# Performance work log

Measured on AMD Instinct MI355X. Metric: run time of the kernel, lower is better.

Reference implementation:

```python
import jax, jax.numpy as jnp
import numpy as np

N_NODES = 100000
N_EDGES = 1600000


def setup_inputs() -> dict:
    key = jax.random.key(0)
    ks = jax.random.split(key, 8)
    in_f, hid, out_c = 128, 128, 64
    return {
        "x": jax.random.normal(ks[0], (N_NODES, in_f), jnp.float32),
        "W_self1": jax.random.normal(ks[1], (in_f, hid), jnp.float32) * 0.05,
        "W_neigh1": jax.random.normal(ks[2], (in_f, hid), jnp.float32) * 0.05,
        "b1": jnp.zeros((hid,), jnp.float32),
        "W_self2": jax.random.normal(ks[3], (hid, out_c), jnp.float32) * 0.05,
        "W_neigh2": jax.random.normal(ks[4], (hid, out_c), jnp.float32) * 0.05,
        "b2": jnp.zeros((out_c,), jnp.float32),
        "src": jax.random.randint(ks[5], (N_EDGES,), 0, N_NODES, jnp.int32),
        "dst": jax.random.randint(ks[6], (N_EDGES,), 0, N_NODES, jnp.int32),
    }


def _sage_conv(h, src, dst, inv_deg, W_self, W_neigh, b):
    # mean aggregation over incoming neighbors: gather + segment-sum + normalize
    agg = jax.ops.segment_sum(h[src], dst, num_segments=N_NODES) * inv_deg  # [N, d]
    return h @ W_self + agg @ W_neigh + b


def reference(x, W_self1, W_neigh1, b1, W_self2, W_neigh2, b2, src, dst):
    # in-degree, clamped to 1 as in DGL SAGEConv
    deg = jax.ops.segment_sum(jnp.ones((N_EDGES,), x.dtype), dst, num_segments=N_NODES)
    inv_deg = (1.0 / jnp.maximum(deg, 1.0))[:, None]  # [N, 1]

    h1 = _sage_conv(x, src, dst, inv_deg, W_self1, W_neigh1, b1)      # conv1
    h1_relu = jax.nn.relu(h1)
    h2 = _sage_conv(h1_relu, src, dst, inv_deg, W_self2, W_neigh2, b2)  # conv2
    # original returns (h, middle_feat=[h1, relu(h1), h2])
    return (h2, h1, h1_relu, h2)
```

## Files before the change

kernel.cpp:

```cpp
#include <hip/hip_runtime.h>
#include <hip/hip_bf16.h>


#define NFEAT 128

typedef __bf16 bf16x8 __attribute__((ext_vector_type(8)));
typedef float  f32x4  __attribute__((ext_vector_type(4)));
typedef unsigned short ushort8v __attribute__((ext_vector_type(8)));

static __device__ inline unsigned short f2bf(float f) {
    union { float f; unsigned int u; } v; v.f = f;
    unsigned int u = v.u;
    unsigned int r = (u + 0x7FFFu + ((u >> 16) & 1u)) >> 16;
    return (unsigned short)r;
}
static __device__ inline float bf2f(unsigned short h) {
    union { unsigned int u; float f; } v; v.u = ((unsigned int)h) << 16;
    return v.f;
}

__global__ __launch_bounds__(256) void k_deg(const int* __restrict__ dst,
                                             int* __restrict__ deg,
                                             int E, int P) {
    int part = blockIdx.x & 7;
    int slice = blockIdx.x >> 3;
    int nslices = gridDim.x >> 3;
    int per = (E + nslices - 1) / nslices;
    int beg = slice * per;
    int end = beg + per; if (end > E) end = E;
    int lo = part * P;
    int hi = lo + P;
    for (int e = beg + threadIdx.x; e < end; e += 256) {
        int d = dst[e];
        if (d >= lo && d < hi) atomicAdd(&deg[d], 1);
    }
}

__global__ __launch_bounds__(256) void k_scan1(const int* __restrict__ deg,
                                               int* __restrict__ escan,
                                               int* __restrict__ bsum, int n) {
    __shared__ int ws4[4];
    int tid = threadIdx.x;
    int base = blockIdx.x * 1024 + tid * 4;
    int d[4];
    #pragma unroll
    for (int j = 0; j < 4; ++j) d[j] = (base + j < n) ? deg[base + j] : 0;
    int s = d[0] + d[1] + d[2] + d[3];
    int lane = tid & 63, wid = tid >> 6;
    int incl = s;
    #pragma unroll
    for (int off = 1; off < 64; off <<= 1) {
        int t = __shfl_up(incl, off, 64);
        if (lane >= off) incl += t;
    }
    if (lane == 63) ws4[wid] = incl;
    __syncthreads();
    int wbase = 0;
    #pragma unroll
    for (int w = 0; w < 4; ++w) if (w < wid) wbase += ws4[w];
    int run = wbase + incl - s;
    #pragma unroll
    for (int j = 0; j < 4; ++j) {
        if (base + j < n) escan[base + j] = run;
        run += d[j];
    }
    if (tid == 255) bsum[blockIdx.x] = run;
}

__global__ __launch_bounds__(1024) void k_scan2(int* __restrict__ bsum, int nb) {
    __shared__ int ws16[16];
    int tid = threadIdx.x;
    int lane = tid & 63, wid = tid >> 6;
    int v = (tid < nb) ? bsum[tid] : 0;
    int incl = v;
    #pragma unroll
    for (int off = 1; off < 64; off <<= 1) {
        int t = __shfl_up(incl, off, 64);
        if (lane >= off) incl += t;
    }
    if (lane == 63) ws16[wid] = incl;
    __syncthreads();
    int wbase = 0;
    for (int w = 0; w < 16; ++w) if (w < wid) wbase += ws16[w];
    if (tid < nb) bsum[tid] = wbase + incl - v;
}

__global__ __launch_bounds__(256) void k_scan3(const int* __restrict__ deg,
                                               const int* __restrict__ escan,
                                               const int* __restrict__ bsum,
                                               int* __restrict__ offs,
                                               int* __restrict__ cursor,
                                               float* __restrict__ invd, int n) {
    int tid = threadIdx.x;
    int base = blockIdx.x * 1024 + tid * 4;
    int bb = bsum[blockIdx.x];
    #pragma unroll
    for (int j = 0; j < 4; ++j) {
        int i = base + j;
        if (i < n) {
            int d = deg[i];
            int off = escan[i] + bb;
            offs[i] = off;
            cursor[i] = off;
            invd[i] = 1.0f / fmaxf((float)d, 1.0f);
            if (i == n - 1) offs[n] = off + d;
        }
    }
}

__global__ __launch_bounds__(256) void k_prep(const float* __restrict__ x,
                                              unsigned short* __restrict__ xb,
                                              const float* __restrict__ Ws1,
                                              const float* __restrict__ Wn1,
                                              unsigned short* __restrict__ wb1,
                                              const float* __restrict__ Ws2,
                                              const float* __restrict__ Wn2,
                                              unsigned short* __restrict__ wb2,
                                              int total4, int C) {
    int b = blockIdx.x;
    if (b < C) {
        int i = b * 256 + threadIdx.x;
        if (i >= total4) return;
        float4 v = *(const float4*)(x + (size_t)i * 4);
        ushort4 o;
        o.x = f2bf(v.x); o.y = f2bf(v.y); o.z = f2bf(v.z); o.w = f2bf(v.w);
        *(ushort4*)(xb + (size_t)i * 4) = o;
    } else if (b < C + 128) {
        int idx = (b - C) * 256 + threadIdx.x;
        int j = idx & 7, lane = (idx >> 3) & 63, ct = (idx >> 9) & 7, ks = idx >> 12;
        int k = ks * 32 + ((lane >> 4) & 3) * 8 + j;
        int n = ct * 16 + (lane & 15);
        float v = (k < 128) ? Ws1[k * 128 + n] : Wn1[(k - 128) * 128 + n];
        wb1[idx] = f2bf(v);
    } else {
        int idx = (b - C - 128) * 256 + threadIdx.x;
        int j = idx & 7, lane = (idx >> 3) & 63, ct = (idx >> 9) & 7, ks = idx >> 12;
        int k = ks * 32 + ((lane >> 4) & 3) * 8 + j;
        int n = ct * 16 + (lane & 15);
        float v = (n < 64) ? Ws2[k * 64 + n] : Wn2[k * 64 + (n - 64)];
        wb2[idx] = f2bf(v);
    }
}

__global__ __launch_bounds__(256) void k_scatter(const int* __restrict__ src,
                                                 const int* __restrict__ dst,
                                                 int* __restrict__ cursor,
                                                 int* __restrict__ ssrc,
                                                 int E, int P) {
    int part = blockIdx.x & 7;
    int slice = blockIdx.x >> 3;
    int nslices = gridDim.x >> 3;
    int per = (E + nslices - 1) / nslices;
    int beg = slice * per;
    int end = beg + per; if (end > E) end = E;
    int lo = part * P;
    int hi = lo + P;
    for (int e = beg + threadIdx.x; e < end; e += 256) {
        int d = dst[e];
        if (d >= lo && d < hi) {
            int pos = atomicAdd(&cursor[d], 1);
            ssrc[pos] = src[e];
        }
    }
}

__global__ __launch_bounds__(256) void k_mmf(const unsigned short* __restrict__ xb,
                                             const int* __restrict__ offs,
                                             const int* __restrict__ ssrc,
                                             const float* __restrict__ invd,
                                             const unsigned short* __restrict__ wb,
                                             const float* __restrict__ bias,
                                             const unsigned short* __restrict__ wb2,
                                             float* __restrict__ h1,
                                             float* __restrict__ h1r,
                                             float* __restrict__ s2,
                                             unsigned short* __restrict__ p2b,
                                             int M) {
    __shared__ unsigned short lh[64 * 128];
    int wave = threadIdx.x >> 6, lane = threadIdx.x & 63;
    int rowbase = blockIdx.x * 64 + wave * 16;
    int node = rowbase + (lane & 15);
    if (node >= M) node = M - 1;
    int q = (lane >> 4) & 3;
    int kq = q * 8;

    float a0[8], a1[8], a2[8], a3[8];
    #pragma unroll
    for (int jj = 0; jj < 8; ++jj) { a0[jj]=0.f; a1[jj]=0.f; a2[jj]=0.f; a3[jj]=0.f; }
    int beg = offs[node], end = offs[node + 1];
    int e = beg;
    for (; e + 2 <= end; e += 2) {
        int s0 = ssrc[e], s1 = ssrc[e + 1];
        const unsigned short* r0p = xb + (size_t)s0 * NFEAT + kq;
        const unsigned short* r1p = xb + (size_t)s1 * NFEAT + kq;
        ushort8v u0 = *(const ushort8v*)(r0p);
        ushort8v u1 = *(const ushort8v*)(r0p + 32);
        ushort8v u2 = *(const ushort8v*)(r0p + 64);
        ushort8v u3 = *(const ushort8v*)(r0p + 96);
        ushort8v w0 = *(const ushort8v*)(r1p);
        ushort8v w1 = *(const ushort8v*)(r1p + 32);
        ushort8v w2 = *(const ushort8v*)(r1p + 64);
        ushort8v w3 = *(const ushort8v*)(r1p + 96);
        #pragma unroll
        for (int jj = 0; jj < 8; ++jj) {
            a0[jj] += bf2f(u0[jj]) + bf2f(w0[jj]);
            a1[jj] += bf2f(u1[jj]) + bf2f(w1[jj]);
            a2[jj] += bf2f(u2[jj]) + bf2f(w2[jj]);
            a3[jj] += bf2f(u3[jj]) + bf2f(w3[jj]);
        }
    }
    if (e < end) {
        int s0 = ssrc[e];
        const unsigned short* rp = xb + (size_t)s0 * NFEAT + kq;
        ushort8v u0 = *(const ushort8v*)(rp);
        ushort8v u1 = *(const ushort8v*)(rp + 32);
        ushort8v u2 = *(const ushort8v*)(rp + 64);
        ushort8v u3 = *(const ushort8v*)(rp + 96);
        #pragma unroll
        for (int jj = 0; jj < 8; ++jj) {
            a0[jj] += bf2f(u0[jj]);
            a1[jj] += bf2f(u1[jj]);
            a2[jj] += bf2f(u2[jj]);
            a3[jj] += bf2f(u3[jj]);
        }
    }
    float iv = invd[node];
    ushort8v g0, g1, g2, g3;
    #pragma unroll
    for (int jj = 0; jj < 8; ++jj) {
        g0[jj] = f2bf(a0[jj] * iv); g1[jj] = f2bf(a1[jj] * iv);
        g2[jj] = f2bf(a2[jj] * iv); g3[jj] = f2bf(a3[jj] * iv);
    }
    bf16x8 ag0 = *(bf16x8*)&g0;
    bf16x8 ag1 = *(bf16x8*)&g1;
    bf16x8 ag2 = *(bf16x8*)&g2;
    bf16x8 ag3 = *(bf16x8*)&g3;

    f32x4 acc[8];
    #pragma unroll
    for (int ct = 0; ct < 8; ++ct) acc[ct] = (f32x4){0.f, 0.f, 0.f, 0.f};

    #pragma unroll 1
    for (int ks = 0; ks < 4; ++ks) {
        bf16x8 a = *(const bf16x8*)(xb + (size_t)node * NFEAT + ks * 32 + kq);
        const unsigned short* wp = wb + ((size_t)ks * 512 + lane) * 8;
        #pragma unroll
        for (int ct = 0; ct < 8; ++ct) {
            bf16x8 b = *(const bf16x8*)(wp + (size_t)ct * 512);
            acc[ct] = __builtin_amdgcn_mfma_f32_16x16x32_bf16(a, b, acc[ct], 0, 0, 0);
        }
    }
    {
        const unsigned short* wl = wb + (size_t)lane * 8;
        #pragma unroll
        for (int ct = 0; ct < 8; ++ct)
            acc[ct] = __builtin_amdgcn_mfma_f32_16x16x32_bf16(
                ag0, *(const bf16x8*)(wl + (size_t)4 * 4096 + ct * 512), acc[ct], 0, 0, 0);
        #pragma unroll
        for (int ct = 0; ct < 8; ++ct)
            acc[ct] = __builtin_amdgcn_mfma_f32_16x16x32_bf16(
                ag1, *(const bf16x8*)(wl + (size_t)5 * 4096 + ct * 512), acc[ct], 0, 0, 0);
        #pragma unroll
        for (int ct = 0; ct < 8; ++ct)
            acc[ct] = __builtin_amdgcn_mfma_f32_16x16x32_bf16(
                ag2, *(const bf16x8*)(wl + (size_t)6 * 4096 + ct * 512), acc[ct], 0, 0, 0);
        #pragma unroll
        for (int ct = 0; ct < 8; ++ct)
            acc[ct] = __builtin_amdgcn_mfma_f32_16x16x32_bf16(
                ag3, *(const bf16x8*)(wl + (size_t)7 * 4096 + ct * 512), acc[ct], 0, 0, 0);
    }

    int r0 = rowbase + q * 4;
    int lr0 = wave * 16 + q * 4;
    int col0 = lane & 15;
    #pragma unroll
    for (int ct = 0; ct < 8; ++ct) {
        int col = ct * 16 + col0;
        float bv = bias[col];
        #pragma unroll
        for (int i = 0; i < 4; ++i) {
            int row = r0 + i;
            float v = acc[ct][i] + bv;
            float vr = fmaxf(v, 0.f);
            int lr = lr0 + i;
            lh[(lr * 128 + col) ^ ((lr & 7) << 3)] = f2bf(vr);
            if (row < M) {
                size_t o = (size_t)row * 128 + col;
                __builtin_nontemporal_store(v, &h1[o]);
                __builtin_nontemporal_store(vr, &h1r[o]);
            }
        }
    }
    __syncthreads();

    f32x4 acc2[8];
    #pragma unroll
    for (int ct = 0; ct < 8; ++ct) acc2[ct] = (f32x4){0.f, 0.f, 0.f, 0.f};
    int lr = wave * 16 + (lane & 15);
    #pragma unroll 1
    for (int ks = 0; ks < 4; ++ks) {
        int ui = (lr * 128 + ks * 32 + kq) ^ ((lr & 7) << 3);
        bf16x8 a = *(const bf16x8*)&lh[ui];
        const unsigned short* wp = wb2 + ((size_t)ks * 512 + lane) * 8;
        #pragma unroll
        for (int ct = 0; ct < 8; ++ct) {
            bf16x8 b = *(const bf16x8*)(wp + (size_t)ct * 512);
            acc2[ct] = __builtin_amdgcn_mfma_f32_16x16x32_bf16(a, b, acc2[ct], 0, 0, 0);
        }
    }
    #pragma unroll
    for (int ct = 0; ct < 8; ++ct) {
        int col = ct * 16 + col0;
        #pragma unroll
        for (int i = 0; i < 4; ++i) {
            int row = r0 + i;
            if (row < M) {
                float v = acc2[ct][i];
                if (col < 64)
                    s2[(size_t)row * 64 + col] = v;
                else
                    p2b[(size_t)row * 64 + (col - 64)] = f2bf(v);
            }
        }
    }
}

__global__ __launch_bounds__(256) void k_agg2(const unsigned short* __restrict__ p2b,
                                              const int* __restrict__ offs,
                                              const int* __restrict__ ssrc,
                                              const float* __restrict__ invd,
                                              const float* __restrict__ s2,
                                              const float* __restrict__ b2,
                                              float* __restrict__ h2a,
                                              float* __restrict__ h2b, int n) {
    int node = blockIdx.x * 16 + (threadIdx.x >> 4);
    if (node >= n) return;
    int lane = threadIdx.x & 15;
    int beg = offs[node], end = offs[node + 1];
    float p0 = 0.f, p1 = 0.f, p2 = 0.f, p3 = 0.f;
    float q0 = 0.f, q1 = 0.f, q2 = 0.f, q3 = 0.f;
    float r0 = 0.f, r1 = 0.f, r2 = 0.f, r3 = 0.f;
    float t0 = 0.f, t1 = 0.f, t2 = 0.f, t3 = 0.f;
    int e = beg;
    for (; e + 8 <= end; e += 8) {
        int s0 = ssrc[e + 0], s1 = ssrc[e + 1], s2i = ssrc[e + 2], s3 = ssrc[e + 3];
        int s4 = ssrc[e + 4], s5 = ssrc[e + 5], s6 = ssrc[e + 6], s7 = ssrc[e + 7];
        ushort4 v0 = *(const ushort4*)(p2b + (size_t)s0 * 64 + lane * 4);
        ushort4 v1 = *(const ushort4*)(p2b + (size_t)s1 * 64 + lane * 4);
        ushort4 v2 = *(const ushort4*)(p2b + (size_t)s2i * 64 + lane * 4);
        ushort4 v3 = *(const ushort4*)(p2b + (size_t)s3 * 64 + lane * 4);
        ushort4 v4 = *(const ushort4*)(p2b + (size_t)s4 * 64 + lane * 4);
        ushort4 v5 = *(const ushort4*)(p2b + (size_t)s5 * 64 + lane * 4);
        ushort4 v6 = *(const ushort4*)(p2b + (size_t)s6 * 64 + lane * 4);
        ushort4 v7 = *(const ushort4*)(p2b + (size_t)s7 * 64 + lane * 4);
        p0 += bf2f(v0.x); p1 += bf2f(v0.y); p2 += bf2f(v0.z); p3 += bf2f(v0.w);
        q0 += bf2f(v1.x); q1 += bf2f(v1.y); q2 += bf2f(v1.z); q3 += bf2f(v1.w);
        r0 += bf2f(v2.x); r1 += bf2f(v2.y); r2 += bf2f(v2.z); r3 += bf2f(v2.w);
        t0 += bf2f(v3.x); t1 += bf2f(v3.y); t2 += bf2f(v3.z); t3 += bf2f(v3.w);
        p0 += bf2f(v4.x); p1 += bf2f(v4.y); p2 += bf2f(v4.z); p3 += bf2f(v4.w);
        q0 += bf2f(v5.x); q1 += bf2f(v5.y); q2 += bf2f(v5.z); q3 += bf2f(v5.w);
        r0 += bf2f(v6.x); r1 += bf2f(v6.y); r2 += bf2f(v6.z); r3 += bf2f(v6.w);
        t0 += bf2f(v7.x); t1 += bf2f(v7.y); t2 += bf2f(v7.z); t3 += bf2f(v7.w);
    }
    for (; e + 4 <= end; e += 4) {
        int s0 = ssrc[e + 0], s1 = ssrc[e + 1], s2i = ssrc[e + 2], s3 = ssrc[e + 3];
        ushort4 v0 = *(const ushort4*)(p2b + (size_t)s0 * 64 + lane * 4);
        ushort4 v1 = *(const ushort4*)(p2b + (size_t)s1 * 64 + lane * 4);
        ushort4 v2 = *(const ushort4*)(p2b + (size_t)s2i * 64 + lane * 4);
        ushort4 v3 = *(const ushort4*)(p2b + (size_t)s3 * 64 + lane * 4);
        p0 += bf2f(v0.x); p1 += bf2f(v0.y); p2 += bf2f(v0.z); p3 += bf2f(v0.w);
        q0 += bf2f(v1.x); q1 += bf2f(v1.y); q2 += bf2f(v1.z); q3 += bf2f(v1.w);
        r0 += bf2f(v2.x); r1 += bf2f(v2.y); r2 += bf2f(v2.z); r3 += bf2f(v2.w);
        t0 += bf2f(v3.x); t1 += bf2f(v3.y); t2 += bf2f(v3.z); t3 += bf2f(v3.w);
    }
    for (; e < end; ++e) {
        int s = ssrc[e];
        ushort4 v = *(const ushort4*)(p2b + (size_t)s * 64 + lane * 4);
        p0 += bf2f(v.x); p1 += bf2f(v.y); p2 += bf2f(v.z); p3 += bf2f(v.w);
    }
    float a0 = (p0 + q0) + (r0 + t0);
    float a1 = (p1 + q1) + (r1 + t1);
    float a2 = (p2 + q2) + (r2 + t2);
    float a3 = (p3 + q3) + (r3 + t3);
    float iv = invd[node];
    float4 sv = *(const float4*)(s2 + (size_t)node * 64 + lane * 4);
    float4 bv = *(const float4*)(b2 + lane * 4);
    f32x4 r;
    r[0] = sv.x + a0 * iv + bv.x;
    r[1] = sv.y + a1 * iv + bv.y;
    r[2] = sv.z + a2 * iv + bv.z;
    r[3] = sv.w + a3 * iv + bv.w;
    __builtin_nontemporal_store(r, (f32x4*)(h2a + (size_t)node * 64 + lane * 4));
    __builtin_nontemporal_store(r, (f32x4*)(h2b + (size_t)node * 64 + lane * 4));
}

static inline size_t align256(size_t x) { return (x + 255) & ~(size_t)255; }

extern "C" void kernel_launch(void* const* d_in, const int* in_sizes, int n_in,
                              void* d_out, int out_size, void* d_ws, size_t ws_size,
                              hipStream_t stream) {
    const float* x   = (const float*)d_in[0];
    const float* Ws1 = (const float*)d_in[1];
    const float* Wn1 = (const float*)d_in[2];
    const float* b1  = (const float*)d_in[3];
    const float* Ws2 = (const float*)d_in[4];
    const float* Wn2 = (const float*)d_in[5];
    const float* b2  = (const float*)d_in[6];
    const int* src   = (const int*)d_in[7];
    const int* dst   = (const int*)d_in[8];

    int E = in_sizes[7];
    int N = in_sizes[0] / NFEAT;

    float* out = (float*)d_out;
    float* h2a = out;
    float* h1  = out + (size_t)N * 64;
    float* h1r = out + (size_t)N * 192;
    float* h2b = out + (size_t)N * 320;

    char* ws = (char*)d_ws;
    size_t off = 0;
    int*   deg    = (int*)(ws + off);  off = align256(off + (size_t)4 * N);
    int*   offs   = (int*)(ws + off);  off = align256(off + (size_t)4 * (N + 1));
    int*   cursor = (int*)(ws + off);  off = align256(off + (size_t)4 * N);
    float* invd   = (float*)(ws + off); off = align256(off + (size_t)4 * N);
    int*   escan  = (int*)(ws + off);  off = align256(off + (size_t)4 * N);
    int*   bsum   = (int*)(ws + off);  off = align256(off + (size_t)4 * 1024);
    int*   ssrc   = (int*)(ws + off);  off = align256(off + (size_t)4 * E);
    unsigned short* wb1 = (unsigned short*)(ws + off); off = align256(off + 2 * 32768);
    unsigned short* wb2 = (unsigned short*)(ws + off); off = align256(off + 2 * 16384);
    unsigned short* xb = (unsigned short*)(ws + off);
    off = align256(off + (size_t)N * NFEAT * 2);
    float* s2 = (float*)(ws + off);
    off = align256(off + (size_t)N * 64 * 4);
    unsigned short* p2b = (unsigned short*)(ws + off);
    off = align256(off + (size_t)N * 64 * 2);

    int nb = (N + 1023) / 1024;
    int P = (N + 7) / 8;
    int C = (N * 32 + 255) / 256;

    hipMemsetAsync(deg, 0, (size_t)4 * N, stream);
    k_deg<<<8 * 256, 256, 0, stream>>>(dst, deg, E, P);
    k_scan1<<<nb, 256, 0, stream>>>(deg, escan, bsum, N);
    k_scan2<<<1, 1024, 0, stream>>>(bsum, nb);
    k_scan3<<<nb, 256, 0, stream>>>(deg, escan, bsum, offs, cursor, invd, N);
    k_prep<<<C + 192, 256, 0, stream>>>(x, xb, Ws1, Wn1, wb1, Ws2, Wn2, wb2,
                                        N * 32, C);
    k_scatter<<<8 * 256, 256, 0, stream>>>(src, dst, cursor, ssrc, E, P);

    k_mmf<<<(N + 63) / 64, 256, 0, stream>>>(xb, offs, ssrc, invd, wb1, b1, wb2,
                                             h1, h1r, s2, p2b, N);
    k_agg2<<<(N + 15) / 16, 256, 0, stream>>>(p2b, offs, ssrc, invd, s2, b2, h2a, h2b, N);
}
```

Measured before the change: 504.3 us.

## Sort nodes by in-degree bucket to balance per-wave aggregation work

Measured after the change: 783.1 us. 1.55x slower.

```diff
diff --git a/kernel.cpp b/kernel.cpp
--- a/kernel.cpp
+++ b/kernel.cpp
@@ -90,8 +90,12 @@
                                                const int* __restrict__ bsum,
                                                int* __restrict__ offs,
                                                int* __restrict__ cursor,
-                                               float* __restrict__ invd, int n) {
+                                               float* __restrict__ invd,
+                                               int* __restrict__ hist, int n) {
+    __shared__ int lhist[256];
     int tid = threadIdx.x;
+    lhist[tid] = 0;
+    __syncthreads();
     int base = blockIdx.x * 1024 + tid * 4;
     int bb = bsum[blockIdx.x];
     #pragma unroll
@@ -103,8 +107,23 @@
             offs[i] = off;
             cursor[i] = off;
             invd[i] = 1.0f / fmaxf((float)d, 1.0f);
+            atomicAdd(&lhist[d < 255 ? d : 255], 1);
             if (i == n - 1) offs[n] = off + d;
         }
+    }
+    __syncthreads();
+    int c = lhist[tid];
+    if (c) atomicAdd(&hist[tid], c);
+}
+
+__global__ __launch_bounds__(256) void k_place(const int* __restrict__ deg,
+                                               int* __restrict__ hist,
+                                               int* __restrict__ perm, int n) {
+    int i = blockIdx.x * 256 + threadIdx.x;
+    if (i < n) {
+        int b = deg[i]; if (b > 255) b = 255;
+        int pos = atomicAdd(&hist[b], 1);
+        perm[pos] = i;
     }
 }
 
@@ -168,6 +187,7 @@
                                              const int* __restrict__ offs,
                                              const int* __restrict__ ssrc,
                                              const float* __restrict__ invd,
+                                             const int* __restrict__ perm,
                                              const unsigned short* __restrict__ wb,
                                              const float* __restrict__ bias,
                                              const unsigned short* __restrict__ wb2,
@@ -179,8 +199,8 @@
     __shared__ unsigned short lh[64 * 128];
     int wave = threadIdx.x >> 6, lane = threadIdx.x & 63;
     int rowbase = blockIdx.x * 64 + wave * 16;
-    int node = rowbase + (lane & 15);
-    if (node >= M) node = M - 1;
+    int pos = rowbase + (lane & 15);
+    int node = perm[pos < M ? pos : M - 1];
     int q = (lane >> 4) & 3;
     int kq = q * 8;
 
@@ -271,6 +291,11 @@
     }
 
     int r0 = rowbase + q * 4;
+    int orow[4];
+    #pragma unroll
+    for (int i = 0; i < 4; ++i)
+        orow[i] = (r0 + i < M) ? perm[r0 + i] : -1;
+
     int lr0 = wave * 16 + q * 4;
     int col0 = lane & 15;
     #pragma unroll
@@ -279,13 +304,12 @@
         float bv = bias[col];
         #pragma unroll
         for (int i = 0; i < 4; ++i) {
-            int row = r0 + i;
             float v = acc[ct][i] + bv;
             float vr = fmaxf(v, 0.f);
             int lr = lr0 + i;
             lh[(lr * 128 + col) ^ ((lr & 7) << 3)] = f2bf(vr);
-            if (row < M) {
-                size_t o = (size_t)row * 128 + col;
+            if (orow[i] >= 0) {
+                size_t o = (size_t)orow[i] * 128 + col;
                 __builtin_nontemporal_store(v, &h1[o]);
                 __builtin_nontemporal_store(vr, &h1r[o]);
             }
@@ -313,13 +337,12 @@
         int col = ct * 16 + col0;
         #pragma unroll
         for (int i = 0; i < 4; ++i) {
-            int row = r0 + i;
-            if (row < M) {
+            if (orow[i] >= 0) {
                 float v = acc2[ct][i];
                 if (col < 64)
-                    s2[(size_t)row * 64 + col] = v;
+                    s2[(size_t)orow[i] * 64 + col] = v;
                 else
-                    p2b[(size_t)row * 64 + (col - 64)] = f2bf(v);
+                    p2b[(size_t)orow[i] * 64 + (col - 64)] = f2bf(v);
             }
         }
     }
@@ -329,12 +352,14 @@
                                               const int* __restrict__ offs,
                                               const int* __restrict__ ssrc,
                                               const float* __restrict__ invd,
+                                              const int* __restrict__ perm,
                                               const float* __restrict__ s2,
                                               const float* __restrict__ b2,
                                               float* __restrict__ h2a,
                                               float* __restrict__ h2b, int n) {
-    int node = blockIdx.x * 16 + (threadIdx.x >> 4);
-    if (node >= n) return;
+    int pos = blockIdx.x * 16 + (threadIdx.x >> 4);
+    if (pos >= n) return;
+    int node = perm[pos];
     int lane = threadIdx.x & 15;
     int beg = offs[node], end = offs[node + 1];
     float p0 = 0.f, p1 = 0.f, p2 = 0.f, p3 = 0.f;
@@ -426,6 +451,8 @@
     float* invd   = (float*)(ws + off); off = align256(off + (size_t)4 * N);
     int*   escan  = (int*)(ws + off);  off = align256(off + (size_t)4 * N);
     int*   bsum   = (int*)(ws + off);  off = align256(off + (size_t)4 * 1024);
+    int*   hist   = (int*)(ws + off);  off = align256(off + (size_t)4 * 256);
+    int*   perm   = (int*)(ws + off);  off = align256(off + (size_t)4 * N);
     int*   ssrc   = (int*)(ws + off);  off = align256(off + (size_t)4 * E);
     unsigned short* wb1 = (unsigned short*)(ws + off); off = align256(off + 2 * 32768);
     unsigned short* wb2 = (unsigned short*)(ws + off); off = align256(off + 2 * 16384);
@@ -441,15 +468,19 @@
     int C = (N * 32 + 255) / 256;
 
     hipMemsetAsync(deg, 0, (size_t)4 * N, stream);
+    hipMemsetAsync(hist, 0, (size_t)4 * 256, stream);
     k_deg<<<8 * 256, 256, 0, stream>>>(dst, deg, E, P);
     k_scan1<<<nb, 256, 0, stream>>>(deg, escan, bsum, N);
     k_scan2<<<1, 1024, 0, stream>>>(bsum, nb);
-    k_scan3<<<nb, 256, 0, stream>>>(deg, escan, bsum, offs, cursor, invd, N);
+    k_scan3<<<nb, 256, 0, stream>>>(deg, escan, bsum, offs, cursor, invd, hist, N);
+    k_scan2<<<1, 256, 0, stream>>>(hist, 256);
+    k_place<<<(N + 255) / 256, 256, 0, stream>>>(deg, hist, perm, N);
     k_prep<<<C + 192, 256, 0, stream>>>(x, xb, Ws1, Wn1, wb1, Ws2, Wn2, wb2,
                                         N * 32, C);
     k_scatter<<<8 * 256, 256, 0, stream>>>(src, dst, cursor, ssrc, E, P);
 
-    k_mmf<<<(N + 63) / 64, 256, 0, stream>>>(xb, offs, ssrc, invd, wb1, b1, wb2,
-                                             h1, h1r, s2, p2b, N);
-    k_agg2<<<(N + 15) / 16, 256, 0, stream>>>(p2b, offs, ssrc, invd, s2, b2, h2a, h2b, N);
-}
+    k_mmf<<<(N + 63) / 64, 256, 0, stream>>>(xb, offs, ssrc, invd, perm, wb1, b1,
+                                             wb2, h1, h1r, s2, p2b, N);
+    k_agg2<<<(N + 15) / 16, 256, 0, stream>>>(p2b, offs, ssrc, invd, perm, s2, b2,
+                                              h2a, h2b, N);
+}
```
